# Performance work log

Measured on AMD Instinct MI355X. Metric: run time of the kernel, lower is better.

Reference implementation:

```python
import jax, jax.numpy as jnp
import numpy as np

B, S, W = 32, 128, 20
WV, CV = 50000, 128
WD, CE = 300, 50
KS = (2, 3, 4, 5)
NF = 64
TOTF = NF * len(KS)
CF = 300
H = 512
L = 9
LP = L + 2
START, END = L, L + 1
NEG = -10000.0


def setup_inputs():
    key = jax.random.key(0)
    ks = jax.random.split(key, 40)
    def nrm(i, shape, scale=0.1):
        return jax.random.normal(ks[i], shape, dtype=jnp.float32) * scale
    inp = {}
    inp['token_ids'] = jax.random.randint(ks[0], (B, S), 0, WV)
    inp['char_ids'] = jax.random.randint(ks[1], (B, S, W), 0, CV)
    lens = jnp.sort(jax.random.randint(ks[2], (B,), S // 2, S + 1))[::-1]
    inp['lens'] = lens.astype(jnp.int32)
    inp['labels'] = jax.random.randint(ks[3], (B, S), 0, L)
    inp['word_embed'] = nrm(4, (WV, WD))
    inp['char_embed'] = nrm(5, (CV, CE))
    for j, k in enumerate(KS):
        inp['conv_w%d' % k] = nrm(6 + j, (k, CE, NF))
        inp['conv_b%d' % k] = nrm(10 + j, (NF,))
    inp['ff_w'] = nrm(14, (CF, TOTF))
    inp['ff_b'] = nrm(15, (CF,))
    inp['wgate_w'] = nrm(16, (WD, WD))
    inp['cgate_w'] = nrm(17, (CF, CF))
    inp['gate_w'] = nrm(18, (WD, WD))
    inp['wih_f'] = nrm(19, (4 * H, WD))
    inp['whh_f'] = nrm(20, (4 * H, H))
    inp['b_f'] = nrm(21, (4 * H,))
    inp['wih_b'] = nrm(22, (4 * H, WD))
    inp['whh_b'] = nrm(23, (4 * H, H))
    inp['b_b'] = nrm(24, (4 * H,))
    inp['out_w'] = nrm(25, (L, 2 * H))
    inp['out_b'] = nrm(26, (L,))
    inp['trn'] = nrm(27, (LP, LP))
    return inp


def _char_cnn(char_ids, char_embed, convs):
    x = char_embed[char_ids.reshape(-1, W)]  # [B*S, W, CE]
    feats = []
    for w, b in convs:
        y = jax.lax.conv_general_dilated(x, w, (1,), 'VALID',
                                         dimension_numbers=('NWC', 'WIO', 'NWC')) + b
        feats.append(jnp.max(jax.nn.relu(y), axis=1))  # max over time -> [B*S, NF]
    return jnp.concatenate(feats, axis=1)  # [B*S, TOTF]


def _run_lstm(x, mask, wih, whh, b, reverse):
    # x [B,S,D], mask bool [B,S]; padded steps freeze state and emit zeros (packed-seq semantics)
    xg = jnp.einsum('bsd,gd->bsg', x, wih) + b  # [B,S,4H]
    xg_t = jnp.swapaxes(xg, 0, 1)               # [S,B,4H]
    m_t = jnp.swapaxes(mask, 0, 1)[..., None]   # [S,B,1]
    h0 = jnp.zeros((x.shape[0], H), x.dtype)
    def step(carry, inp):
        h, c = carry
        g_t, m = inp
        g = g_t + h @ whh.T
        i, f, gg, o = jnp.split(g, 4, axis=-1)  # torch gate order i,f,g,o
        cn = jax.nn.sigmoid(f) * c + jax.nn.sigmoid(i) * jnp.tanh(gg)
        hn = jax.nn.sigmoid(o) * jnp.tanh(cn)
        h = jnp.where(m, hn, h)
        c = jnp.where(m, cn, c)
        return (h, c), jnp.where(m, hn, 0.0)
    _, out = jax.lax.scan(step, (h0, h0), (xg_t, m_t), reverse=reverse)
    return jnp.swapaxes(out, 0, 1)  # [B,S,H]


def _crf_norm(logits, mask, trn):
    # logits [B,S,LP]; trn[i,j] = score(prev=j -> next=i)
    alpha = logits[:, 0] + trn[:, START][None, :]
    lt = jnp.swapaxes(logits, 0, 1)[1:]                 # [S-1,B,LP]
    mt = jnp.swapaxes(mask, 0, 1)[1:][..., None]        # [S-1,B,1]
    def step(alpha, inp):
        lg, m = inp
        new = jax.scipy.special.logsumexp(alpha[:, None, :] + trn[None], axis=2) + lg
        return jnp.where(m, new, alpha), None
    alpha, _ = jax.lax.scan(step, alpha, (lt, mt))
    return jax.scipy.special.logsumexp(alpha + trn[END][None, :], axis=1)


def _crf_gold(logits, labels, lens, mask, trn):
    fm = mask.astype(logits.dtype)
    emit = jnp.take_along_axis(logits, labels[..., None], axis=2)[..., 0]
    emit = jnp.sum(emit * fm, axis=1)
    trans = trn[labels[:, 1:], labels[:, :-1]] * fm[:, 1:]
    first = trn[labels[:, 0], START]
    last_lab = jnp.take_along_axis(labels, (lens - 1)[:, None], axis=1)[:, 0]
    return emit + jnp.sum(trans, axis=1) + first + trn[END, last_lab]


def reference(token_ids, char_ids, lens, labels, word_embed, char_embed,
              conv_w2, conv_b2, conv_w3, conv_b3, conv_w4, conv_b4, conv_w5, conv_b5,
              ff_w, ff_b, wgate_w, cgate_w, gate_w,
              wih_f, whh_f, b_f, wih_b, whh_b, b_b, out_w, out_b, trn):
    word_in = word_embed[token_ids]                               # [B,S,WD]
    convs = [(conv_w2, conv_b2), (conv_w3, conv_b3), (conv_w4, conv_b4), (conv_w5, conv_b5)]
    ch = _char_cnn(char_ids, char_embed, convs)                   # [B*S,TOTF]
    char_in = (ch @ ff_w.T + ff_b).reshape(B, S, CF)              # CharCNNFF output
    g = jax.nn.sigmoid(jnp.tanh(word_in @ wgate_w.T + char_in @ cgate_w.T) @ gate_w.T)
    feats = g * word_in + (1.0 - g) * char_in                     # gated fusion (dropout = eval identity)
    mask = jnp.arange(S)[None, :] < lens[:, None]                 # [B,S] bool
    hf = _run_lstm(feats, mask, wih_f, whh_f, b_f, False)
    hb = _run_lstm(feats, mask, wih_b, whh_b, b_b, True)
    lstm_out = jnp.concatenate([hf, hb], axis=-1)                 # [B,S,2H]
    logits = lstm_out @ out_w.T + out_b                           # [B,S,L]
    pads = jnp.full((B, S, 2), NEG, logits.dtype)
    logits = jnp.concatenate([logits, pads], axis=2)              # pad_logits -> [B,S,LP]
    norm = _crf_norm(logits, mask, trn)
    gold = _crf_gold(logits, labels, lens, mask, trn)
    loglik = gold - norm
    return (loglik, logits)
```

## Files before the change

### kernel.cpp

```cpp
#include <hip/hip_runtime.h>

#define NB    32
#define SEQ   128
#define WCH   20
#define CED   50
#define NFLT  64
#define WDIM  300
#define HD    512
#define NWORD 4096
#define LPAD  11
#define NEGV  -10000.0f
#define LSTM_BLOCKS 16

typedef float f32x4 __attribute__((ext_vector_type(4)));
typedef float f32x16 __attribute__((ext_vector_type(16)));
typedef __bf16 bf16x8 __attribute__((ext_vector_type(8)));
typedef unsigned short u16x8 __attribute__((ext_vector_type(8)));
typedef unsigned short u16x4 __attribute__((ext_vector_type(4)));
typedef unsigned long long ull;

static __device__ __forceinline__ unsigned short f2bf(float f) {
  unsigned u = __builtin_bit_cast(unsigned, f);
  u += 0x7fffu + ((u >> 16) & 1u);
  return (unsigned short)(u >> 16);
}
static __device__ __forceinline__ float bf2f(unsigned short s) {
  unsigned u = ((unsigned)s) << 16;
  return __builtin_bit_cast(float, u);
}
static __device__ __forceinline__ float sigf(float x) { return 1.0f / (1.0f + expf(-x)); }

__global__ __launch_bounds__(256) void conv_kernel(
    const int* __restrict__ char_ids, const float* __restrict__ char_embed,
    const float* __restrict__ w2, const float* __restrict__ b2,
    const float* __restrict__ w3, const float* __restrict__ b3,
    const float* __restrict__ w4, const float* __restrict__ b4,
    const float* __restrict__ w5, const float* __restrict__ b5,
    float* __restrict__ ch)
{
  __shared__ __align__(16) float xT[CED][WCH];
  int wi = blockIdx.x;
  int tid = threadIdx.x;
  for (int e = tid; e < WCH * CED; e += 256) {
    int p = e / CED, c = e - p * CED;
    int cid = char_ids[wi * WCH + p];
    xT[c][p] = char_embed[cid * CED + c];
  }
  __syncthreads();
  int w = tid >> 6, f = tid & 63;
  int k = w + 2;
  int P = WCH - k + 1;
  const float* cw = (w == 0) ? w2 : (w == 1) ? w3 : (w == 2) ? w4 : w5;
  const float* cb = (w == 0) ? b2 : (w == 1) ? b3 : (w == 2) ? b4 : b5;
  float acc[19];
  #pragma unroll
  for (int p = 0; p < 19; p++) acc[p] = 0.f;
  for (int c = 0; c < CED; c++) {
    float xr[20];
    const float4* rowp = (const float4*)&xT[c][0];
    #pragma unroll
    for (int q = 0; q < 5; q++) {
      float4 v = rowp[q];
      xr[4*q+0] = v.x; xr[4*q+1] = v.y; xr[4*q+2] = v.z; xr[4*q+3] = v.w;
    }
    #pragma unroll
    for (int dw = 0; dw < 5; dw++) {
      if (dw < k) {
        float wv = cw[(dw * CED + c) * NFLT + f];
        #pragma unroll
        for (int p = 0; p < 19; p++) {
          if (p < P) acc[p] += xr[p + dw] * wv;
        }
      }
    }
  }
  float m = acc[0];
  #pragma unroll
  for (int p = 1; p < 19; p++) if (p < P) m = fmaxf(m, acc[p]);
  ch[wi * 256 + w * 64 + f] = fmaxf(0.f, m + cb[f]);
}

__global__ void gather_word_kernel(const int* __restrict__ token_ids,
                                   const float* __restrict__ word_embed,
                                   float* __restrict__ word_in)
{
  int idx = blockIdx.x * 256 + threadIdx.x;
  if (idx < NWORD * WDIM) {
    int i = idx / WDIM, c = idx - i * WDIM;
    word_in[idx] = word_embed[token_ids[i] * WDIM + c];
  }
}

__global__ __launch_bounds__(256) void gemm_bt_kernel(
    const float* __restrict__ A, const float* __restrict__ Bw,
    const float* __restrict__ bias, const float* __restrict__ Cin,
    float* __restrict__ Cout, unsigned short* __restrict__ Cbf,
    int M, int N, int K, int act, int gridN)
{
  __shared__ __align__(16) unsigned short As[128 * 32];
  __shared__ __align__(16) unsigned short Bs[128 * 32];
  int bid = blockIdx.x;
  int tm = bid / gridN, tn = bid - tm * gridN;
  int m0 = tm * 128, n0 = tn * 128;
  int tid = threadIdx.x;
  int lane = tid & 63, w = tid >> 6;
  int wr = (w >> 1) * 64, wc = (w & 1) * 64;
  f32x4 acc[4][4] = {};
  int fr = lane & 15, fk = (lane >> 4) * 8;

  for (int k0 = 0; k0 < K; k0 += 32) {
    __syncthreads();
    #pragma unroll
    for (int i = 0; i < 4; i++) {
      int idx = tid + i * 256;
      int r = idx >> 3, c4 = idx & 7;
      int kx = k0 + c4 * 4;
      int ra = m0 + r, rb = n0 + r;
      f32x4 av = {0.f,0.f,0.f,0.f}, bv = {0.f,0.f,0.f,0.f};
      if (kx < K) {
        if (ra < M) av = *(const f32x4*)&A[(size_t)ra * K + kx];
        if (rb < N) bv = *(const f32x4*)&Bw[(size_t)rb * K + kx];
      }
      u16x4 ap, bp;
      #pragma unroll
      for (int j = 0; j < 4; j++) { ap[j] = f2bf(av[j]); bp[j] = f2bf(bv[j]); }
      *(u16x4*)&As[r * 32 + c4 * 4] = ap;
      *(u16x4*)&Bs[r * 32 + c4 * 4] = bp;
    }
    __syncthreads();
    bf16x8 a[4], b[4];
    #pragma unroll
    for (int mt = 0; mt < 4; mt++)
      a[mt] = *(const bf16x8*)&As[(wr + mt * 16 + fr) * 32 + fk];
    #pragma unroll
    for (int nt = 0; nt < 4; nt++)
      b[nt] = *(const bf16x8*)&Bs[(wc + nt * 16 + fr) * 32 + fk];
    #pragma unroll
    for (int mt = 0; mt < 4; mt++)
      #pragma unroll
      for (int nt = 0; nt < 4; nt++)
        acc[mt][nt] = __builtin_amdgcn_mfma_f32_16x16x32_bf16(a[mt], b[nt], acc[mt][nt], 0, 0, 0);
  }

  #pragma unroll
  for (int mt = 0; mt < 4; mt++) {
    #pragma unroll
    for (int nt = 0; nt < 4; nt++) {
      #pragma unroll
      for (int j = 0; j < 4; j++) {
        int row = m0 + wr + mt * 16 + (lane >> 4) * 4 + j;
        int col = n0 + wc + nt * 16 + (lane & 15);
        if (row < M && col < N) {
          float v = acc[mt][nt][j];
          if (Cin)  v += Cin[(size_t)row * N + col];
          if (bias) v += bias[col];
          if (act == 1)      v = tanhf(v);
          else if (act == 2) v = sigf(v);
          if (Cbf) Cbf[(size_t)row * N + col] = f2bf(v);
          else     Cout[(size_t)row * N + col] = v;
        }
      }
    }
  }
}

__global__ void feats_kernel(const float* __restrict__ g, const float* __restrict__ word_in,
                             const float* __restrict__ char_in, float* __restrict__ feats,
                             unsigned* __restrict__ flags)
{
  if (blockIdx.x == 0 && threadIdx.x < 32)
    __hip_atomic_store(&flags[threadIdx.x], 0u, __ATOMIC_RELAXED, __HIP_MEMORY_SCOPE_AGENT);
  int idx = blockIdx.x * 256 + threadIdx.x;
  if (idx < NWORD * WDIM) {
    float gg = g[idx];
    feats[idx] = gg * word_in[idx] + (1.f - gg) * char_in[idx];
  }
}

__global__ __launch_bounds__(512, 2) void lstm_kernel(
    const unsigned short* __restrict__ xg_f, const unsigned short* __restrict__ xg_b,
    const float* __restrict__ whh_f, const float* __restrict__ whh_b,
    const int* __restrict__ lens,
    float* __restrict__ lstm_out, unsigned short* __restrict__ h_glob,
    unsigned* __restrict__ flags)
{
  int sl = blockIdx.x;
  int hs0 = sl << 5;
  int tid = threadIdx.x, lane = tid & 63, w = tid >> 6;
  int g = w & 3, kh = w >> 2;
  int l31 = lane & 31, le = lane >> 5;

  unsigned short* hgF = h_glob;
  unsigned short* hgB = h_glob + 2 * NB * HD;

  bf16x8 wfF[16], wfB[16];
  {
    const float* sF = whh_f + (size_t)(g * HD + hs0 + l31) * HD + kh * 256 + le * 8;
    const float* sB = whh_b + (size_t)(g * HD + hs0 + l31) * HD + kh * 256 + le * 8;
    #pragma unroll
    for (int kk = 0; kk < 16; kk++) {
      u16x8 tf_, tb_;
      #pragma unroll
      for (int j = 0; j < 8; j++) { tf_[j] = f2bf(sF[kk * 16 + j]); tb_[j] = f2bf(sB[kk * 16 + j]); }
      wfF[kk] = __builtin_bit_cast(bf16x8, tf_);
      wfB[kk] = __builtin_bit_cast(bf16x8, tb_);
    }
  }

  __shared__ __align__(16) unsigned short hS[16384];
  __shared__ float Gs[2][NB][132];

  int b = tid >> 4, up = tid & 15;
  int srow = tid >> 4, sq = tid & 15;
  int mylen = lens[b];
  float cF[2] = {0.f,0.f}, hpF[2] = {0.f,0.f};
  float cB[2] = {0.f,0.f}, hpB[2] = {0.f,0.f};

  ull hr[8];

  auto stage_issue = [&](const unsigned short* hbuf) {
    const ull* hq = (const ull*)hbuf;
    #pragma unroll
    for (int i = 0; i < 8; i++)
      hr[i] = __hip_atomic_load(hq + srow * 128 + sq * 8 + i, __ATOMIC_RELAXED, __HIP_MEMORY_SCOPE_AGENT);
  };
  auto stage_write = [&]() {
    int rs = ((srow ^ (sq & 7)) & 31) << 4;
    #pragma unroll
    for (int e2 = 0; e2 < 4; e2++) {
      int kk = 2 * sq + (e2 >> 1), e = e2 & 1;
      uint4 qv;
      qv.x = (unsigned)hr[2*e2];   qv.y = (unsigned)(hr[2*e2] >> 32);
      qv.z = (unsigned)hr[2*e2+1]; qv.w = (unsigned)(hr[2*e2+1] >> 32);
      *(uint4*)((char*)hS + (((kk * 2 + e) << 9) + rs)) = qv;
    }
  };
  auto wait_flags = [&](int base, unsigned target) {
    if (tid == 0) {
      const ull* fp = (const ull*)(flags + base);
      for (;;) {
        unsigned mn = 0xffffffffu;
        #pragma unroll
        for (int i = 0; i < 8; i++) {
          ull v = __hip_atomic_load(fp + i, __ATOMIC_RELAXED, __HIP_MEMORY_SCOPE_AGENT);
          unsigned a = (unsigned)v, bq = (unsigned)(v >> 32);
          mn = a < mn ? a : mn; mn = bq < mn ? bq : mn;
        }
        if (mn >= target) break;
        __builtin_amdgcn_s_sleep(1);
      }
    }
  };

  unsigned xF[4], xB[4];
  {
    const unsigned* pF = (const unsigned*)xg_f;
    const unsigned* pB = (const unsigned*)xg_b;
    size_t oF = (size_t)(b * SEQ + 0) * 1024 + (hs0 >> 1) + up;
    size_t oB = (size_t)(b * SEQ + (SEQ - 1)) * 1024 + (hs0 >> 1) + up;
    #pragma unroll
    for (int g4 = 0; g4 < 4; g4++) { xF[g4] = pF[oF + g4 * 256]; xB[g4] = pB[oB + g4 * 256]; }
  }

  for (int s = 0; s < SEQ; s++) {
    int tf_ = s, tb_ = SEQ - 1 - s;
    if (s > 0) stage_write();
    __syncthreads();
    {
      f32x16 acc = {};
      if (s > 0) {
        #pragma unroll
        for (int q = 0; q < 16; q++) {
          int kk = kh * 16 + q;
          int rs = ((l31 ^ ((kk >> 1) & 7)) & 31) << 4;
          bf16x8 a = *(const bf16x8*)((const char*)hS + (((kk * 2 + le) << 9) + rs));
          acc = __builtin_amdgcn_mfma_f32_32x32x16_bf16(a, wfF[q], acc, 0, 0, 0);
        }
      }
      #pragma unroll
      for (int r = 0; r < 16; r++) {
        int row = (r & 3) + 8 * (r >> 2) + 4 * le;
        Gs[kh][row][g * 32 + l31] = acc[r];
      }
    }
    if (s > 0) wait_flags(16, (unsigned)s);
    __syncthreads();
    if (s > 0) stage_issue(hgB + (s & 1) * (NB * HD));
    {
      bool mk = (tf_ < mylen);
      float pre[4][2];
      #pragma unroll
      for (int g4 = 0; g4 < 4; g4++) {
        float2 p0 = *(const float2*)&Gs[0][b][g4 * 32 + 2 * up];
        float2 p1 = *(const float2*)&Gs[1][b][g4 * 32 + 2 * up];
        pre[g4][0] = p0.x + p1.x; pre[g4][1] = p0.y + p1.y;
      }
      float2 ov; unsigned pk = 0;
      #pragma unroll
      for (int j = 0; j < 2; j++) {
        float xi = bf2f((unsigned short)(xF[0] >> (16*j)));
        float xf = bf2f((unsigned short)(xF[1] >> (16*j)));
        float xG = bf2f((unsigned short)(xF[2] >> (16*j)));
        float xo = bf2f((unsigned short)(xF[3] >> (16*j)));
        float iv = sigf(xi + pre[0][j]);
        float fv = sigf(xf + pre[1][j]);
        float Gv = tanhf(xG + pre[2][j]);
        float o_ = sigf(xo + pre[3][j]);
        float cn = fv * cF[j] + iv * Gv;
        float hh = o_ * tanhf(cn);
        if (mk) cF[j] = cn;
        float hk = mk ? hh : hpF[j];
        hpF[j] = hk;
        (&ov.x)[j] = mk ? hh : 0.f;
        pk |= ((unsigned)f2bf(hk)) << (16*j);
      }
      size_t ob = (size_t)(b * SEQ + tf_) * 1024 + hs0 + 2 * up;
      *(float2*)&lstm_out[ob] = ov;
      unsigned* hd = (unsigned*)(hgF + ((s & 1) ^ 1) * (NB * HD));
      __hip_atomic_store(&hd[(b * HD + hs0 + 2 * up) >> 1], pk, __ATOMIC_RELAXED, __HIP_MEMORY_SCOPE_AGENT);
    }
    __syncthreads();
    if (tid == 0)
      __hip_atomic_store(&flags[sl], (unsigned)(s + 1), __ATOMIC_RELAXED, __HIP_MEMORY_SCOPE_AGENT);
    if (s + 1 < SEQ) {
      const unsigned* pF = (const unsigned*)xg_f;
      size_t oF = (size_t)(b * SEQ + (s + 1)) * 1024 + (hs0 >> 1) + up;
      #pragma unroll
      for (int g4 = 0; g4 < 4; g4++) xF[g4] = pF[oF + g4 * 256];
    }
    if (s > 0) stage_write();
    __syncthreads();
    {
      f32x16 acc = {};
      if (s > 0) {
        #pragma unroll
        for (int q = 0; q < 16; q++) {
          int kk = kh * 16 + q;
          int rs = ((l31 ^ ((kk >> 1) & 7)) & 31) << 4;
          bf16x8 a = *(const bf16x8*)((const char*)hS + (((kk * 2 + le) << 9) + rs));
          acc = __builtin_amdgcn_mfma_f32_32x32x16_bf16(a, wfB[q], acc, 0, 0, 0);
        }
      }
      #pragma unroll
      for (int r = 0; r < 16; r++) {
        int row = (r & 3) + 8 * (r >> 2) + 4 * le;
        Gs[kh][row][g * 32 + l31] = acc[r];
      }
    }
    if (s + 1 < SEQ) wait_flags(0, (unsigned)(s + 1));
    __syncthreads();
    if (s + 1 < SEQ) stage_issue(hgF + ((s + 1) & 1) * (NB * HD));
    {
      bool mk = (tb_ < mylen);
      float pre[4][2];
      #pragma unroll
      for (int g4 = 0; g4 < 4; g4++) {
        float2 p0 = *(const float2*)&Gs[0][b][g4 * 32 + 2 * up];
        float2 p1 = *(const float2*)&Gs[1][b][g4 * 32 + 2 * up];
        pre[g4][0] = p0.x + p1.x; pre[g4][1] = p0.y + p1.y;
      }
      float2 ov; unsigned pk = 0;
      #pragma unroll
      for (int j = 0; j < 2; j++) {
        float xi = bf2f((unsigned short)(xB[0] >> (16*j)));
        float xf = bf2f((unsigned short)(xB[1] >> (16*j)));
        float xG = bf2f((unsigned short)(xB[2] >> (16*j)));
        float xo = bf2f((unsigned short)(xB[3] >> (16*j)));
        float iv = sigf(xi + pre[0][j]);
        float fv = sigf(xf + pre[1][j]);
        float Gv = tanhf(xG + pre[2][j]);
        float o_ = sigf(xo + pre[3][j]);
        float cn = fv * cB[j] + iv * Gv;
        float hh = o_ * tanhf(cn);
        if (mk) cB[j] = cn;
        float hk = mk ? hh : hpB[j];
        hpB[j] = hk;
        (&ov.x)[j] = mk ? hh : 0.f;
        pk |= ((unsigned)f2bf(hk)) << (16*j);
      }
      size_t ob = (size_t)(b * SEQ + tb_) * 1024 + HD + hs0 + 2 * up;
      *(float2*)&lstm_out[ob] = ov;
      unsigned* hd = (unsigned*)(hgB + ((s & 1) ^ 1) * (NB * HD));
      __hip_atomic_store(&hd[(b * HD + hs0 + 2 * up) >> 1], pk, __ATOMIC_RELAXED, __HIP_MEMORY_SCOPE_AGENT);
    }
    __syncthreads();
    if (tid == 0)
      __hip_atomic_store(&flags[16 + sl], (unsigned)(s + 1), __ATOMIC_RELAXED, __HIP_MEMORY_SCOPE_AGENT);
    if (s + 1 < SEQ) {
      const unsigned* pB = (const unsigned*)xg_b;
      size_t oB = (size_t)(b * SEQ + (SEQ - 2 - s)) * 1024 + (hs0 >> 1) + up;
      #pragma unroll
      for (int g4 = 0; g4 < 4; g4++) xB[g4] = pB[oB + g4 * 256];
    }
  }
}

__global__ __launch_bounds__(64) void logits_kernel(
    const float* __restrict__ lstm_out, const float* __restrict__ out_w,
    const float* __restrict__ out_b, float* __restrict__ lg)
{
  int rw = blockIdx.x, j = threadIdx.x;
  const float* row = lstm_out + (size_t)rw * 1024;
  float s[9];
  #pragma unroll
  for (int l = 0; l < 9; l++) s[l] = 0.f;
  for (int e = j; e < 1024; e += 64) {
    float x = row[e];
    #pragma unroll
    for (int l = 0; l < 9; l++) s[l] += x * out_w[l * 1024 + e];
  }
  #pragma unroll
  for (int l = 0; l < 9; l++) {
    #pragma unroll
    for (int off = 32; off > 0; off >>= 1) s[l] += __shfl_xor(s[l], off);
  }
  float v = NEGV;
  if (j < 9) {
    float r = (j==0)?s[0]:(j==1)?s[1]:(j==2)?s[2]:(j==3)?s[3]:(j==4)?s[4]:
              (j==5)?s[5]:(j==6)?s[6]:(j==7)?s[7]:s[8];
    v = r + out_b[j];
  }
  if (j < LPAD) lg[(size_t)rw * LPAD + j] = v;
}

__global__ __launch_bounds__(64) void crf_gold_kernel(
    const float* __restrict__ lg, const int* __restrict__ labels,
    const int* __restrict__ lens, const float* __restrict__ trn, float* __restrict__ gold)
{
  int b = blockIdx.x, j = threadIdx.x;
  int len = lens[b];
  const int* lab = labels + b * SEQ;
  const float* l0 = lg + (size_t)b * SEQ * LPAD;
  float s = 0.f;
  for (int t = j; t < SEQ; t += 64) {
    if (t < len) {
      s += l0[t * LPAD + lab[t]];
      if (t >= 1) s += trn[lab[t] * LPAD + lab[t - 1]];
    }
  }
  #pragma unroll
  for (int off = 32; off > 0; off >>= 1) s += __shfl_xor(s, off);
  if (j == 0) {
    s += trn[lab[0] * LPAD + 9];
    s += trn[10 * LPAD + lab[len - 1]];
    gold[b] = s;
  }
}

__global__ __launch_bounds__(64) void crf_norm_kernel(
    const float* __restrict__ lg, const int* __restrict__ lens,
    const float* __restrict__ trn, const float* __restrict__ gold, float* __restrict__ out_ll)
{
  int b = blockIdx.x, i = threadIdx.x;
  int len = lens[b];
  const float* l0 = lg + (size_t)b * SEQ * LPAD;
  bool act = (i < LPAD);
  float trow[LPAD];
  #pragma unroll
  for (int jj = 0; jj < LPAD; jj++) trow[jj] = act ? trn[i * LPAD + jj] : 0.f;
  float alpha = act ? (l0[i] + trow[9]) : -1e30f;

  for (int t = 1; t < SEQ; t++) {
    float vj[LPAD];
    #pragma unroll
    for (int jj = 0; jj < LPAD; jj++) vj[jj] = __shfl(alpha, jj) + trow[jj];
    float mx = vj[0];
    #pragma unroll
    for (int jj = 1; jj < LPAD; jj++) mx = fmaxf(mx, vj[jj]);
    float sum = 0.f;
    #pragma unroll
    for (int jj = 0; jj < LPAD; jj++) sum += expf(vj[jj] - mx);
    float lgv = act ? l0[t * LPAD + i] : 0.f;
    float nw = mx + logf(sum) + lgv;
    if (act && t < len) alpha = nw;
  }
  float vj[LPAD];
  #pragma unroll
  for (int jj = 0; jj < LPAD; jj++) vj[jj] = __shfl(alpha, jj) + trn[10 * LPAD + jj];
  float mx = vj[0];
  #pragma unroll
  for (int jj = 1; jj < LPAD; jj++) mx = fmaxf(mx, vj[jj]);
  float sum = 0.f;
  #pragma unroll
  for (int jj = 0; jj < LPAD; jj++) sum += expf(vj[jj] - mx);
  if (i == 0) out_ll[b] = gold[b] - (mx + logf(sum));
}

extern "C" void kernel_launch(void* const* d_in, const int* in_sizes, int n_in,
                              void* d_out, int out_size, void* d_ws, size_t ws_size,
                              hipStream_t stream)
{
  (void)in_sizes; (void)n_in; (void)out_size; (void)ws_size;
  const int*   token_ids = (const int*)d_in[0];
  const int*   char_ids  = (const int*)d_in[1];
  const int*   lens      = (const int*)d_in[2];
  const int*   labels    = (const int*)d_in[3];
  const float* word_embed= (const float*)d_in[4];
  const float* char_embed= (const float*)d_in[5];
  const float* w2 = (const float*)d_in[6];  const float* cb2 = (const float*)d_in[7];
  const float* w3 = (const float*)d_in[8];  const float* cb3 = (const float*)d_in[9];
  const float* w4 = (const float*)d_in[10]; const float* cb4 = (const float*)d_in[11];
  const float* w5 = (const float*)d_in[12]; const float* cb5 = (const float*)d_in[13];
  const float* ff_w = (const float*)d_in[14]; const float* ff_b = (const float*)d_in[15];
  const float* wgate_w = (const float*)d_in[16];
  const float* cgate_w = (const float*)d_in[17];
  const float* gate_w  = (const float*)d_in[18];
  const float* wih_f = (const float*)d_in[19]; const float* whh_f = (const float*)d_in[20];
  const float* b_f   = (const float*)d_in[21];
  const float* wih_b = (const float*)d_in[22]; const float* whh_b = (const float*)d_in[23];
  const float* b_b   = (const float*)d_in[24];
  const float* out_w = (const float*)d_in[25]; const float* out_b = (const float*)d_in[26];
  const float* trn   = (const float*)d_in[27];

  char* ws = (char*)d_ws;
  size_t off = 0;
  auto alloc = [&](size_t bytes) { void* p = ws + off; off += (bytes + 255) & ~(size_t)255; return p; };
  float* ch       = (float*)alloc((size_t)NWORD * 256 * 4);
  float* word_in  = (float*)alloc((size_t)NWORD * WDIM * 4);
  float* char_in  = (float*)alloc((size_t)NWORD * WDIM * 4);
  float* t1       = (float*)alloc((size_t)NWORD * WDIM * 4);
  float* gbuf     = (float*)alloc((size_t)NWORD * WDIM * 4);
  float* feats    = (float*)alloc((size_t)NWORD * WDIM * 4);
  unsigned short* xgf = (unsigned short*)alloc((size_t)NWORD * 2048 * 2);
  unsigned short* xgb = (unsigned short*)alloc((size_t)NWORD * 2048 * 2);
  float* lstm_o   = (float*)alloc((size_t)NWORD * 1024 * 4);
  unsigned short* hglob = (unsigned short*)alloc((size_t)2 * 2 * NB * HD * 2);
  float* gold     = (float*)alloc((size_t)NB * 4);
  unsigned* flags = (unsigned*)alloc(256);

  float* outp   = (float*)d_out;
  float* loglik = outp;
  float* logits = outp + NB;

  conv_kernel<<<NWORD, 256, 0, stream>>>(char_ids, char_embed, w2, cb2, w3, cb3, w4, cb4, w5, cb5, ch);
  gather_word_kernel<<<(NWORD * WDIM + 255) / 256, 256, 0, stream>>>(token_ids, word_embed, word_in);
  gemm_bt_kernel<<<32 * 3, 256, 0, stream>>>(ch, ff_w, ff_b, nullptr, char_in, nullptr, NWORD, 300, 256, 0, 3);
  gemm_bt_kernel<<<32 * 3, 256, 0, stream>>>(word_in, wgate_w, nullptr, nullptr, t1, nullptr, NWORD, 300, 300, 0, 3);
  gemm_bt_kernel<<<32 * 3, 256, 0, stream>>>(char_in, cgate_w, nullptr, t1, t1, nullptr, NWORD, 300, 300, 1, 3);
  gemm_bt_kernel<<<32 * 3, 256, 0, stream>>>(t1, gate_w, nullptr, nullptr, gbuf, nullptr, NWORD, 300, 300, 2, 3);
  feats_kernel<<<(NWORD * WDIM + 255) / 256, 256, 0, stream>>>(gbuf, word_in, char_in, feats, flags);
  gemm_bt_kernel<<<32 * 16, 256, 0, stream>>>(feats, wih_f, b_f, nullptr, nullptr, xgf, NWORD, 2048, 300, 0, 16);
  gemm_bt_kernel<<<32 * 16, 256, 0, stream>>>(feats, wih_b, b_b, nullptr, nullptr, xgb, NWORD, 2048, 300, 0, 16);
  {
    void* args[] = { (void*)&xgf, (void*)&xgb, (void*)&whh_f, (void*)&whh_b,
                     (void*)&lens, (void*)&lstm_o, (void*)&hglob, (void*)&flags };
    hipLaunchCooperativeKernel((void*)lstm_kernel, dim3(LSTM_BLOCKS), dim3(512), args, 0, stream);
  }
  logits_kernel<<<NWORD, 64, 0, stream>>>(lstm_o, out_w, out_b, logits);
  crf_gold_kernel<<<NB, 64, 0, stream>>>(logits, labels, lens, trn, gold);
  crf_norm_kernel<<<NB, 64, 0, stream>>>(logits, lens, trn, gold, loglik);
}
```

Baseline: 1.398 ms.

## Replace LSTM LDS staging and block barriers with per-wave flags and history buffer

The LSTM kernel now writes every step's hidden state into a full bf16 history buffer and uses per-wave flags (256 in total), polled by a whole wave with __all. Each wave loads its MFMA A operands straight from global memory into registers, which removes the LDS staging and several __syncthreads per step. The fp32 lstm_out write is dropped, and the logits kernel reads the bf16 history instead, applying the length mask itself. This shortens the serial per-step critical path. In exchange every wave polls global memory, and the logits now come from bf16-rounded hidden states.

Measured after the change: 3.287 ms. 2.35x slower.

```diff
diff --git a/kernel.cpp b/kernel.cpp
--- a/kernel.cpp
+++ b/kernel.cpp
@@ -18,6 +18,7 @@
 typedef unsigned short u16x8 __attribute__((ext_vector_type(8)));
 typedef unsigned short u16x4 __attribute__((ext_vector_type(4)));
 typedef unsigned long long ull;
+typedef unsigned long long ullx2 __attribute__((ext_vector_type(2)));
 
 static __device__ __forceinline__ unsigned short f2bf(float f) {
   unsigned u = __builtin_bit_cast(unsigned, f);
@@ -168,7 +169,7 @@
                              const float* __restrict__ char_in, float* __restrict__ feats,
                              unsigned* __restrict__ flags)
 {
-  if (blockIdx.x == 0 && threadIdx.x < 32)
+  if (blockIdx.x == 0)
     __hip_atomic_store(&flags[threadIdx.x], 0u, __ATOMIC_RELAXED, __HIP_MEMORY_SCOPE_AGENT);
   int idx = blockIdx.x * 256 + threadIdx.x;
   if (idx < NWORD * WDIM) {
@@ -177,12 +178,11 @@
   }
 }
 
-__global__ __launch_bounds__(512, 2) void lstm_kernel(
+__global__ __launch_bounds__(512) void lstm_kernel(
     const unsigned short* __restrict__ xg_f, const unsigned short* __restrict__ xg_b,
     const float* __restrict__ whh_f, const float* __restrict__ whh_b,
     const int* __restrict__ lens,
-    float* __restrict__ lstm_out, unsigned short* __restrict__ h_glob,
-    unsigned* __restrict__ flags)
+    unsigned short* __restrict__ hist, unsigned* __restrict__ flags)
 {
   int sl = blockIdx.x;
   int hs0 = sl << 5;
@@ -190,65 +190,41 @@
   int g = w & 3, kh = w >> 2;
   int l31 = lane & 31, le = lane >> 5;
 
-  unsigned short* hgF = h_glob;
-  unsigned short* hgB = h_glob + 2 * NB * HD;
+  unsigned short* histF = hist;
+  unsigned short* histB = hist + (size_t)SEQ * NB * HD;
+  unsigned* flF = flags;
+  unsigned* flB = flags + 128;
+  int myflag = sl * 8 + w;
 
   bf16x8 wfF[16], wfB[16];
   {
     const float* sF = whh_f + (size_t)(g * HD + hs0 + l31) * HD + kh * 256 + le * 8;
     const float* sB = whh_b + (size_t)(g * HD + hs0 + l31) * HD + kh * 256 + le * 8;
     #pragma unroll
-    for (int kk = 0; kk < 16; kk++) {
+    for (int q = 0; q < 16; q++) {
       u16x8 tf_, tb_;
       #pragma unroll
-      for (int j = 0; j < 8; j++) { tf_[j] = f2bf(sF[kk * 16 + j]); tb_[j] = f2bf(sB[kk * 16 + j]); }
-      wfF[kk] = __builtin_bit_cast(bf16x8, tf_);
-      wfB[kk] = __builtin_bit_cast(bf16x8, tb_);
-    }
-  }
-
-  __shared__ __align__(16) unsigned short hS[16384];
-  __shared__ float Gs[2][NB][132];
+      for (int j = 0; j < 8; j++) { tf_[j] = f2bf(sF[q * 16 + j]); tb_[j] = f2bf(sB[q * 16 + j]); }
+      wfF[q] = __builtin_bit_cast(bf16x8, tf_);
+      wfB[q] = __builtin_bit_cast(bf16x8, tb_);
+    }
+  }
+
+  __shared__ float Gs[2][2][NB][132];
 
   int b = tid >> 4, up = tid & 15;
-  int srow = tid >> 4, sq = tid & 15;
   int mylen = lens[b];
   float cF[2] = {0.f,0.f}, hpF[2] = {0.f,0.f};
   float cB[2] = {0.f,0.f}, hpB[2] = {0.f,0.f};
-
-  ull hr[8];
-
-  auto stage_issue = [&](const unsigned short* hbuf) {
-    const ull* hq = (const ull*)hbuf;
-    #pragma unroll
-    for (int i = 0; i < 8; i++)
-      hr[i] = __hip_atomic_load(hq + srow * 128 + sq * 8 + i, __ATOMIC_RELAXED, __HIP_MEMORY_SCOPE_AGENT);
-  };
-  auto stage_write = [&]() {
-    int rs = ((srow ^ (sq & 7)) & 31) << 4;
-    #pragma unroll
-    for (int e2 = 0; e2 < 4; e2++) {
-      int kk = 2 * sq + (e2 >> 1), e = e2 & 1;
-      uint4 qv;
-      qv.x = (unsigned)hr[2*e2];   qv.y = (unsigned)(hr[2*e2] >> 32);
-      qv.z = (unsigned)hr[2*e2+1]; qv.w = (unsigned)(hr[2*e2+1] >> 32);
-      *(uint4*)((char*)hS + (((kk * 2 + e) << 9) + rs)) = qv;
-    }
-  };
-  auto wait_flags = [&](int base, unsigned target) {
-    if (tid == 0) {
-      const ull* fp = (const ull*)(flags + base);
-      for (;;) {
-        unsigned mn = 0xffffffffu;
-        #pragma unroll
-        for (int i = 0; i < 8; i++) {
-          ull v = __hip_atomic_load(fp + i, __ATOMIC_RELAXED, __HIP_MEMORY_SCOPE_AGENT);
-          unsigned a = (unsigned)v, bq = (unsigned)(v >> 32);
-          mn = a < mn ? a : mn; mn = bq < mn ? bq : mn;
-        }
-        if (mn >= target) break;
-        __builtin_amdgcn_s_sleep(1);
-      }
+  ull af[32];
+
+  auto pollflags = [&](unsigned* fl, unsigned tgt) {
+    const ull* fp = (const ull*)fl;
+    for (;;) {
+      ull v = __hip_atomic_load(fp + lane, __ATOMIC_RELAXED, __HIP_MEMORY_SCOPE_AGENT);
+      bool ok = ((unsigned)v >= tgt) && ((unsigned)(v >> 32) >= tgt);
+      if (__all(ok)) break;
+      __builtin_amdgcn_s_sleep(1);
     }
   };
 
@@ -263,39 +239,45 @@
   }
 
   for (int s = 0; s < SEQ; s++) {
-    int tf_ = s, tb_ = SEQ - 1 - s;
-    if (s > 0) stage_write();
-    __syncthreads();
     {
       f32x16 acc = {};
       if (s > 0) {
         #pragma unroll
         for (int q = 0; q < 16; q++) {
-          int kk = kh * 16 + q;
-          int rs = ((l31 ^ ((kk >> 1) & 7)) & 31) << 4;
-          bf16x8 a = *(const bf16x8*)((const char*)hS + (((kk * 2 + le) << 9) + rs));
-          acc = __builtin_amdgcn_mfma_f32_32x32x16_bf16(a, wfF[q], acc, 0, 0, 0);
+          ullx2 t2 = { af[2*q], af[2*q+1] };
+          acc = __builtin_amdgcn_mfma_f32_32x32x16_bf16(__builtin_bit_cast(bf16x8, t2), wfF[q], acc, 0, 0, 0);
         }
       }
       #pragma unroll
       for (int r = 0; r < 16; r++) {
         int row = (r & 3) + 8 * (r >> 2) + 4 * le;
-        Gs[kh][row][g * 32 + l31] = acc[r];
-      }
-    }
-    if (s > 0) wait_flags(16, (unsigned)s);
-    __syncthreads();
-    if (s > 0) stage_issue(hgB + (s & 1) * (NB * HD));
-    {
-      bool mk = (tf_ < mylen);
+        Gs[0][kh][row][g * 32 + l31] = acc[r];
+      }
+      if (s > 0) {
+        pollflags(flB, (unsigned)s);
+        const ull* base = (const ull*)histB + ((((size_t)(s - 1) * NB + l31) * HD + kh * 256 + le * 8) >> 2);
+        #pragma unroll
+        for (int q = 0; q < 16; q++) {
+          af[2*q]   = __hip_atomic_load(base + q * 4,     __ATOMIC_RELAXED, __HIP_MEMORY_SCOPE_AGENT);
+          af[2*q+1] = __hip_atomic_load(base + q * 4 + 1, __ATOMIC_RELAXED, __HIP_MEMORY_SCOPE_AGENT);
+        }
+      }
+      unsigned xn0 = 0, xn1 = 0, xn2 = 0, xn3 = 0;
+      if (s + 1 < SEQ) {
+        const unsigned* pF = (const unsigned*)xg_f;
+        size_t o = (size_t)(b * SEQ + (s + 1)) * 1024 + (hs0 >> 1) + up;
+        xn0 = pF[o]; xn1 = pF[o + 256]; xn2 = pF[o + 512]; xn3 = pF[o + 768];
+      }
+      __syncthreads();
+      bool mk = (s < mylen);
       float pre[4][2];
       #pragma unroll
       for (int g4 = 0; g4 < 4; g4++) {
-        float2 p0 = *(const float2*)&Gs[0][b][g4 * 32 + 2 * up];
-        float2 p1 = *(const float2*)&Gs[1][b][g4 * 32 + 2 * up];
+        float2 p0 = *(const float2*)&Gs[0][0][b][g4 * 32 + 2 * up];
+        float2 p1 = *(const float2*)&Gs[0][1][b][g4 * 32 + 2 * up];
         pre[g4][0] = p0.x + p1.x; pre[g4][1] = p0.y + p1.y;
       }
-      float2 ov; unsigned pk = 0;
+      unsigned pk = 0;
       #pragma unroll
       for (int j = 0; j < 2; j++) {
         float xi = bf2f((unsigned short)(xF[0] >> (16*j)));
@@ -311,55 +293,56 @@
         if (mk) cF[j] = cn;
         float hk = mk ? hh : hpF[j];
         hpF[j] = hk;
-        (&ov.x)[j] = mk ? hh : 0.f;
         pk |= ((unsigned)f2bf(hk)) << (16*j);
       }
-      size_t ob = (size_t)(b * SEQ + tf_) * 1024 + hs0 + 2 * up;
-      *(float2*)&lstm_out[ob] = ov;
-      unsigned* hd = (unsigned*)(hgF + ((s & 1) ^ 1) * (NB * HD));
-      __hip_atomic_store(&hd[(b * HD + hs0 + 2 * up) >> 1], pk, __ATOMIC_RELAXED, __HIP_MEMORY_SCOPE_AGENT);
-    }
-    __syncthreads();
-    if (tid == 0)
-      __hip_atomic_store(&flags[sl], (unsigned)(s + 1), __ATOMIC_RELAXED, __HIP_MEMORY_SCOPE_AGENT);
-    if (s + 1 < SEQ) {
-      const unsigned* pF = (const unsigned*)xg_f;
-      size_t oF = (size_t)(b * SEQ + (s + 1)) * 1024 + (hs0 >> 1) + up;
-      #pragma unroll
-      for (int g4 = 0; g4 < 4; g4++) xF[g4] = pF[oF + g4 * 256];
-    }
-    if (s > 0) stage_write();
-    __syncthreads();
+      unsigned* hd = (unsigned*)histF;
+      __hip_atomic_store(&hd[(((size_t)s * NB + b) * HD + hs0 + 2 * up) >> 1], pk,
+                         __ATOMIC_RELAXED, __HIP_MEMORY_SCOPE_AGENT);
+      xF[0] = xn0; xF[1] = xn1; xF[2] = xn2; xF[3] = xn3;
+      asm volatile("s_waitcnt vmcnt(0)" ::: "memory");
+      if (lane == 0)
+        __hip_atomic_store(&flF[myflag], (unsigned)(s + 1), __ATOMIC_RELAXED, __HIP_MEMORY_SCOPE_AGENT);
+    }
     {
+      int tb = SEQ - 1 - s;
       f32x16 acc = {};
       if (s > 0) {
         #pragma unroll
         for (int q = 0; q < 16; q++) {
-          int kk = kh * 16 + q;
-          int rs = ((l31 ^ ((kk >> 1) & 7)) & 31) << 4;
-          bf16x8 a = *(const bf16x8*)((const char*)hS + (((kk * 2 + le) << 9) + rs));
-          acc = __builtin_amdgcn_mfma_f32_32x32x16_bf16(a, wfB[q], acc, 0, 0, 0);
+          ullx2 t2 = { af[2*q], af[2*q+1] };
+          acc = __builtin_amdgcn_mfma_f32_32x32x16_bf16(__builtin_bit_cast(bf16x8, t2), wfB[q], acc, 0, 0, 0);
         }
       }
       #pragma unroll
       for (int r = 0; r < 16; r++) {
         int row = (r & 3) + 8 * (r >> 2) + 4 * le;
-        Gs[kh][row][g * 32 + l31] = acc[r];
-      }
-    }
-    if (s + 1 < SEQ) wait_flags(0, (unsigned)(s + 1));
-    __syncthreads();
-    if (s + 1 < SEQ) stage_issue(hgF + ((s + 1) & 1) * (NB * HD));
-    {
-      bool mk = (tb_ < mylen);
+        Gs[1][kh][row][g * 32 + l31] = acc[r];
+      }
+      if (s + 1 < SEQ) {
+        pollflags(flF, (unsigned)(s + 1));
+        const ull* base = (const ull*)histF + ((((size_t)s * NB + l31) * HD + kh * 256 + le * 8) >> 2);
+        #pragma unroll
+        for (int q = 0; q < 16; q++) {
+          af[2*q]   = __hip_atomic_load(base + q * 4,     __ATOMIC_RELAXED, __HIP_MEMORY_SCOPE_AGENT);
+          af[2*q+1] = __hip_atomic_load(base + q * 4 + 1, __ATOMIC_RELAXED, __HIP_MEMORY_SCOPE_AGENT);
+        }
+      }
+      unsigned xn0 = 0, xn1 = 0, xn2 = 0, xn3 = 0;
+      if (s + 1 < SEQ) {
+        const unsigned* pB = (const unsigned*)xg_b;
+        size_t o = (size_t)(b * SEQ + (SEQ - 2 - s)) * 1024 + (hs0 >> 1) + up;
+        xn0 = pB[o]; xn1 = pB[o + 256]; xn2 = pB[o + 512]; xn3 = pB[o + 768];
+      }
+      __syncthreads();
+      bool mk = (tb < mylen);
       float pre[4][2];
       #pragma unroll
       for (int g4 = 0; g4 < 4; g4++) {
-        float2 p0 = *(const float2*)&Gs[0][b][g4 * 32 + 2 * up];
-        float2 p1 = *(const float2*)&Gs[1][b][g4 * 32 + 2 * up];
+        float2 p0 = *(const float2*)&Gs[1][0][b][g4 * 32 + 2 * up];
+        float2 p1 = *(const float2*)&Gs[1][1][b][g4 * 32 + 2 * up];
         pre[g4][0] = p0.x + p1.x; pre[g4][1] = p0.y + p1.y;
       }
-      float2 ov; unsigned pk = 0;
+      unsigned pk = 0;
       #pragma unroll
       for (int j = 0; j < 2; j++) {
         float xi = bf2f((unsigned short)(xB[0] >> (16*j)));
@@ -375,39 +358,43 @@
         if (mk) cB[j] = cn;
         float hk = mk ? hh : hpB[j];
         hpB[j] = hk;
-        (&ov.x)[j] = mk ? hh : 0.f;
         pk |= ((unsigned)f2bf(hk)) << (16*j);
       }
-      size_t ob = (size_t)(b * SEQ + tb_) * 1024 + HD + hs0 + 2 * up;
-      *(float2*)&lstm_out[ob] = ov;
-      unsigned* hd = (unsigned*)(hgB + ((s & 1) ^ 1) * (NB * HD));
-      __hip_atomic_store(&hd[(b * HD + hs0 + 2 * up) >> 1], pk, __ATOMIC_RELAXED, __HIP_MEMORY_SCOPE_AGENT);
-    }
-    __syncthreads();
-    if (tid == 0)
-      __hip_atomic_store(&flags[16 + sl], (unsigned)(s + 1), __ATOMIC_RELAXED, __HIP_MEMORY_SCOPE_AGENT);
-    if (s + 1 < SEQ) {
-      const unsigned* pB = (const unsigned*)xg_b;
-      size_t oB = (size_t)(b * SEQ + (SEQ - 2 - s)) * 1024 + (hs0 >> 1) + up;
-      #pragma unroll
-      for (int g4 = 0; g4 < 4; g4++) xB[g4] = pB[oB + g4 * 256];
+      unsigned* hd = (unsigned*)histB;
+      __hip_atomic_store(&hd[(((size_t)s * NB + b) * HD + hs0 + 2 * up) >> 1], pk,
+                         __ATOMIC_RELAXED, __HIP_MEMORY_SCOPE_AGENT);
+      xB[0] = xn0; xB[1] = xn1; xB[2] = xn2; xB[3] = xn3;
+      asm volatile("s_waitcnt vmcnt(0)" ::: "memory");
+      if (lane == 0)
+        __hip_atomic_store(&flB[myflag], (unsigned)(s + 1), __ATOMIC_RELAXED, __HIP_MEMORY_SCOPE_AGENT);
     }
   }
 }
 
 __global__ __launch_bounds__(64) void logits_kernel(
-    const float* __restrict__ lstm_out, const float* __restrict__ out_w,
-    const float* __restrict__ out_b, float* __restrict__ lg)
+    const unsigned short* __restrict__ hist, const int* __restrict__ lens,
+    const float* __restrict__ out_w, const float* __restrict__ out_b, float* __restrict__ lg)
 {
   int rw = blockIdx.x, j = threadIdx.x;
-  const float* row = lstm_out + (size_t)rw * 1024;
+  int b = rw >> 7, t = rw & 127;
+  bool mk = t < lens[b];
   float s[9];
   #pragma unroll
   for (int l = 0; l < 9; l++) s[l] = 0.f;
-  for (int e = j; e < 1024; e += 64) {
-    float x = row[e];
-    #pragma unroll
-    for (int l = 0; l < 9; l++) s[l] += x * out_w[l * 1024 + e];
+  if (mk) {
+    size_t base = ((size_t)t * NB + b) * HD;
+    const unsigned short* hf = hist + base;
+    const unsigned short* hb = hist + (size_t)SEQ * NB * HD + base;
+    u16x8 vf = *(const u16x8*)&hf[j * 8];
+    u16x8 vb = *(const u16x8*)&hb[j * 8];
+    #pragma unroll
+    for (int k = 0; k < 8; k++) {
+      float xf = bf2f(vf[k]), xb = bf2f(vb[k]);
+      int e = j * 8 + k;
+      #pragma unroll
+      for (int l = 0; l < 9; l++)
+        s[l] += xf * out_w[l * 1024 + e] + xb * out_w[l * 1024 + 512 + e];
+    }
   }
   #pragma unroll
   for (int l = 0; l < 9; l++) {
@@ -523,10 +510,9 @@
   float* feats    = (float*)alloc((size_t)NWORD * WDIM * 4);
   unsigned short* xgf = (unsigned short*)alloc((size_t)NWORD * 2048 * 2);
   unsigned short* xgb = (unsigned short*)alloc((size_t)NWORD * 2048 * 2);
-  float* lstm_o   = (float*)alloc((size_t)NWORD * 1024 * 4);
-  unsigned short* hglob = (unsigned short*)alloc((size_t)2 * 2 * NB * HD * 2);
+  unsigned short* hist = (unsigned short*)alloc((size_t)2 * SEQ * NB * HD * 2);
   float* gold     = (float*)alloc((size_t)NB * 4);
-  unsigned* flags = (unsigned*)alloc(256);
+  unsigned* flags = (unsigned*)alloc(1024);
 
   float* outp   = (float*)d_out;
   float* loglik = outp;
@@ -543,10 +529,10 @@
   gemm_bt_kernel<<<32 * 16, 256, 0, stream>>>(feats, wih_b, b_b, nullptr, nullptr, xgb, NWORD, 2048, 300, 0, 16);
   {
     void* args[] = { (void*)&xgf, (void*)&xgb, (void*)&whh_f, (void*)&whh_b,
-                     (void*)&lens, (void*)&lstm_o, (void*)&hglob, (void*)&flags };
+                     (void*)&lens, (void*)&hist, (void*)&flags };
     hipLaunchCooperativeKernel((void*)lstm_kernel, dim3(LSTM_BLOCKS), dim3(512), args, 0, stream);
   }
-  logits_kernel<<<NWORD, 64, 0, stream>>>(lstm_o, out_w, out_b, logits);
+  logits_kernel<<<NWORD, 64, 0, stream>>>(hist, lens, out_w, out_b, logits);
   crf_gold_kernel<<<NB, 64, 0, stream>>>(logits, labels, lens, trn, gold);
   crf_norm_kernel<<<NB, 64, 0, stream>>>(logits, lens, trn, gold, loglik);
 }
```
